# Optimization experiments

Hardware: AMD Instinct MI355X
Metric: run time of the kernel (lower is better)

The kernel has to match this reference:

```python
import jax, jax.numpy as jnp
import numpy as np

D_MODEL = 4096
NUM_EXPERTS = 64
TOP_K = 8


def setup_inputs() -> dict:
    key = jax.random.key(0)
    kx, kw = jax.random.split(key)
    x = jax.random.normal(kx, (4, 4096, D_MODEL), dtype=jnp.float32)
    # nn.Linear weight [num_experts, d_model]; y = x @ W.T
    W = jax.random.normal(kw, (NUM_EXPERTS, D_MODEL), dtype=jnp.float32) * (1.0 / np.sqrt(D_MODEL))
    return {"x": x, "W": W}


def reference(x, W):
    # logits: [b, s, e]
    logits = jnp.einsum('bsd,ed->bse', x, W)
    router_probs = jax.nn.softmax(logits, axis=-1)
    top_k_weights, top_k_indices = jax.lax.top_k(router_probs, TOP_K)
    top_k_weights = top_k_weights / (jnp.sum(top_k_weights, axis=-1, keepdims=True) + 1e-9)
    return top_k_weights, top_k_indices, router_probs
```

## Files before the change

kernel.cpp:

```cpp
#include <hip/hip_runtime.h>
#include <math.h>

#define D_MODEL 4096
#define NEXP    64
#define TOPK    8
#define NTOK    16384
#define BLK_TOK 64
#define DC      128
#define NCHUNK  (D_MODEL / DC)

#define WT2_FLOATS (NEXP * D_MODEL)

__global__ void transpose_w_kernel(const float* __restrict__ W, float* __restrict__ WT2) {
    int o = blockIdx.x * 256 + threadIdx.x;
    int j = o & 7;
    int d = (o >> 3) & (D_MODEL - 1);
    int g = o >> 15;
    WT2[o] = W[(size_t)(g * 8 + j) * D_MODEL + d];
}

__global__ __launch_bounds__(512)
void router_kernel(const float* __restrict__ x, const float* __restrict__ WT2,
                   float* __restrict__ out_w, float* __restrict__ out_i,
                   float* __restrict__ out_p, int* __restrict__ cnt,
                   int* __restrict__ list) {
    __shared__ float lds_x[2][DC / 4][BLK_TOK][4];

    const int tid  = threadIdx.x;
    const int lane = tid & 63;
    const int g    = __builtin_amdgcn_readfirstlane(tid >> 6);
    const int tok0 = blockIdx.x * BLK_TOK;

    const int row = tid >> 3;
    const int q   = tid & 7;

    float acc[8];
#pragma unroll
    for (int j = 0; j < 8; ++j) acc[j] = 0.f;

    float4 xr[4];
    const float* xbase = x + (size_t)(tok0 + row) * D_MODEL + q * 4;
    const float* wk    = WT2 + (g << 15);

    auto load_chunk = [&](int d0) {
#pragma unroll
        for (int j = 0; j < 4; ++j)
            xr[j] = *(const float4*)(xbase + d0 + j * 32);
    };
    auto store_chunk = [&](int buf) {
#pragma unroll
        for (int j = 0; j < 4; ++j)
            *(float4*)&lds_x[buf][q + j * 8][row][0] = xr[j];
    };
    auto compute_chunk = [&](int buf, int k) {
        const float* wc = wk + k * DC * 8;
        const float* xl = &lds_x[buf][0][lane][0];
#pragma unroll 4
        for (int d4 = 0; d4 < DC / 4; ++d4) {
            const float4 xq = *(const float4*)(xl + d4 * (BLK_TOK * 4));
            const float* wd = wc + d4 * 32;
#pragma unroll
            for (int dd = 0; dd < 4; ++dd) {
                const float xv = (dd == 0) ? xq.x : (dd == 1) ? xq.y : (dd == 2) ? xq.z : xq.w;
#pragma unroll
                for (int j = 0; j < 8; ++j)
                    acc[j] = fmaf(xv, wd[dd * 8 + j], acc[j]);
            }
        }
    };

    load_chunk(0);
    store_chunk(0);
    __syncthreads();

    for (int k = 0; k < NCHUNK; ++k) {
        if (k + 1 < NCHUNK) load_chunk((k + 1) * DC);
        compute_chunk(k & 1, k);
        if (k + 1 < NCHUNK) store_chunk((k + 1) & 1);
        __syncthreads();
    }

    float* lg = (float*)lds_x;
#pragma unroll
    for (int j = 0; j < 8; ++j)
        lg[lane * 65 + g * 8 + j] = acc[j];
    __syncthreads();

    if (tid < 64) {
        const int tok = tok0 + tid;
        float p[64];
        float m = -INFINITY;
#pragma unroll
        for (int e = 0; e < 64; ++e) {
            p[e] = lg[tid * 65 + e];
            m = fmaxf(m, p[e]);
        }
        float z = 0.f;
#pragma unroll
        for (int e = 0; e < 64; ++e) {
            p[e] = __expf(p[e] - m);
            z += p[e];
        }
        const float rz = 1.f / z;
#pragma unroll
        for (int e = 0; e < 64; ++e) {
            p[e] *= rz;
            lg[tid * 65 + e] = p[e];
        }

        float tv[9]; int ti[9];
#pragma unroll
        for (int k = 0; k < 9; ++k) { tv[k] = -1.f; ti[k] = 0; }
        for (int e = 0; e < 64; ++e) {
            float v = p[e]; int idx = e;
#pragma unroll
            for (int k = 0; k < 9; ++k) {
                const bool gt = v > tv[k];
                const float nv = gt ? v : tv[k];
                const int   ni = gt ? idx : ti[k];
                const float ov = gt ? tv[k] : v;
                const int   oi = gt ? ti[k] : idx;
                tv[k] = nv; ti[k] = ni; v = ov; idx = oi;
            }
        }
        int flag = 0;
#pragma unroll
        for (int k = 0; k < 8; ++k)
            if (tv[k] - tv[k + 1] <= tv[k] * 2e-4f + 1e-12f) flag = 1;
        if (flag) {
            int s = atomicAdd(cnt, 1);
            list[s] = tok;
        }

        float s8 = 0.f;
#pragma unroll
        for (int k = 0; k < 8; ++k) s8 += tv[k];
        const float denom = s8 + 1e-9f;
#pragma unroll
        for (int k = 0; k < 8; ++k) {
            out_w[tok * TOPK + k] = tv[k] / denom;
            out_i[tok * TOPK + k] = (float)ti[k];
        }
    }
    __syncthreads();

    for (int i = tid; i < BLK_TOK * 16; i += 512) {
        const int t  = i >> 4;
        const int e4 = (i & 15) << 2;
        const float* src = &lg[t * 65 + e4];
        float4 v = make_float4(src[0], src[1], src[2], src[3]);
        *(float4*)&out_p[(size_t)(tok0 + t) * NEXP + e4] = v;
    }
}

__global__ __launch_bounds__(64)
void repair_kernel(const float* __restrict__ x, const float* __restrict__ W,
                   const int* __restrict__ cnt, const int* __restrict__ list,
                   float* __restrict__ out_w, float* __restrict__ out_i) {
    __shared__ float  xs[D_MODEL];
    __shared__ double ls[NEXP];
    const int tid = threadIdx.x;
    const int n   = cnt[0];

    for (int i = blockIdx.x; i < n; i += gridDim.x) {
        const int tok = list[i];
        __syncthreads();
        const float4* xsrc = (const float4*)(x + (size_t)tok * D_MODEL);
        for (int v = tid; v < D_MODEL / 4; v += 64)
            ((float4*)xs)[v] = xsrc[v];
        __syncthreads();

        const float* wrow = W + (size_t)tid * D_MODEL;
        double s0 = 0., s1 = 0., s2 = 0., s3 = 0.;
        for (int d = 0; d < D_MODEL; d += 4) {
            const float4 wv = *(const float4*)(wrow + d);
            const float4 xv = *(const float4*)(xs + d);
            s0 += (double)xv.x * (double)wv.x;
            s1 += (double)xv.y * (double)wv.y;
            s2 += (double)xv.z * (double)wv.z;
            s3 += (double)xv.w * (double)wv.w;
        }
        ls[tid] = (s0 + s1) + (s2 + s3);
        __syncthreads();

        if (tid == 0) {
            double m = -1e300;
            for (int e = 0; e < 64; ++e) m = ls[e] > m ? ls[e] : m;
            double p[64], Z = 0.;
            for (int e = 0; e < 64; ++e) { p[e] = exp(ls[e] - m); Z += p[e]; }
            for (int e = 0; e < 64; ++e) p[e] /= Z;

            double tv[8]; int ti[8];
            for (int k = 0; k < 8; ++k) { tv[k] = -1.; ti[k] = 0; }
            for (int e = 0; e < 64; ++e) {
                double v = p[e]; int idx = e;
                for (int k = 0; k < 8; ++k) {
                    const bool gt = v > tv[k];
                    const double nv = gt ? v : tv[k];
                    const int    ni = gt ? idx : ti[k];
                    const double ov = gt ? tv[k] : v;
                    const int    oi = gt ? ti[k] : idx;
                    tv[k] = nv; ti[k] = ni; v = ov; idx = oi;
                }
            }
            double s8 = 0.;
            for (int k = 0; k < 8; ++k) s8 += tv[k];
            const double denom = s8 + 1e-9;
            for (int k = 0; k < 8; ++k) {
                out_w[tok * TOPK + k] = (float)(tv[k] / denom);
                out_i[tok * TOPK + k] = (float)ti[k];
            }
        }
    }
}

extern "C" void kernel_launch(void* const* d_in, const int* in_sizes, int n_in,
                              void* d_out, int out_size, void* d_ws, size_t ws_size,
                              hipStream_t stream) {
    const float* x = (const float*)d_in[0];
    const float* W = (const float*)d_in[1];

    float* WT2  = (float*)d_ws;
    int*   cnt  = (int*)((float*)d_ws + WT2_FLOATS);
    int*   list = cnt + 1;

    float* out   = (float*)d_out;
    float* out_w = out;
    float* out_i = out + NTOK * TOPK;
    float* out_p = out + 2 * NTOK * TOPK;

    hipMemsetAsync(cnt, 0, sizeof(int), stream);
    transpose_w_kernel<<<(WT2_FLOATS) / 256, 256, 0, stream>>>(W, WT2);
    router_kernel<<<NTOK / BLK_TOK, 512, 0, stream>>>(x, WT2, out_w, out_i, out_p, cnt, list);
    repair_kernel<<<256, 64, 0, stream>>>(x, W, cnt, list, out_w, out_i);
}
```

Baseline: 658.1 us.

## Split router GEMM over K with atomic logit accumulation and separate finalize kernel

Splits the reduction dimension in two so twice as many blocks run, and each block has 16 waves handling 4 experts each. Partial logits are summed into the probability output buffer with float atomics, and softmax and top-k move to a new finalize kernel. The LDS layout is XOR-swizzled, the inner loop uses packed 2-wide FMAs, and the repair kernel splits each dot product across four waves. In exchange it adds a memset of the output buffer, an extra kernel launch, and atomic traffic on the logits.

Result: slower. 1.478 ms (+124.5%).

```diff
diff --git a/kernel.cpp b/kernel.cpp
--- a/kernel.cpp
+++ b/kernel.cpp
@@ -7,65 +7,76 @@
 #define NTOK    16384
 #define BLK_TOK 64
 #define DC      128
-#define NCHUNK  (D_MODEL / DC)
+#define KSPLIT  2
+#define KHALF   (D_MODEL / KSPLIT)
+#define NCHUNK_H (KHALF / DC)
+#define EPW     4
+#define NWAVE   (NEXP / EPW)
+#define NTHR    (NWAVE * 64)
 
 #define WT2_FLOATS (NEXP * D_MODEL)
+
+typedef float v2f __attribute__((ext_vector_type(2)));
 
 __global__ void transpose_w_kernel(const float* __restrict__ W, float* __restrict__ WT2) {
     int o = blockIdx.x * 256 + threadIdx.x;
-    int j = o & 7;
-    int d = (o >> 3) & (D_MODEL - 1);
-    int g = o >> 15;
-    WT2[o] = W[(size_t)(g * 8 + j) * D_MODEL + d];
-}
-
-__global__ __launch_bounds__(512)
+    int p  = o & 1;
+    int j  = (o >> 1) & 3;
+    int d2 = (o >> 3) & 2047;
+    int g  = o >> 14;
+    WT2[o] = W[(size_t)(g * 4 + j) * D_MODEL + 2 * d2 + p];
+}
+
+__global__ __launch_bounds__(NTHR, 8)
 void router_kernel(const float* __restrict__ x, const float* __restrict__ WT2,
-                   float* __restrict__ out_w, float* __restrict__ out_i,
-                   float* __restrict__ out_p, int* __restrict__ cnt,
-                   int* __restrict__ list) {
-    __shared__ float lds_x[2][DC / 4][BLK_TOK][4];
+                   float* __restrict__ Pacc) {
+    __shared__ __align__(16) float lds[2 * 8192];
 
     const int tid  = threadIdx.x;
     const int lane = tid & 63;
     const int g    = __builtin_amdgcn_readfirstlane(tid >> 6);
-    const int tok0 = blockIdx.x * BLK_TOK;
-
-    const int row = tid >> 3;
-    const int q   = tid & 7;
-
-    float acc[8];
-#pragma unroll
-    for (int j = 0; j < 8; ++j) acc[j] = 0.f;
-
-    float4 xr[4];
-    const float* xbase = x + (size_t)(tok0 + row) * D_MODEL + q * 4;
-    const float* wk    = WT2 + (g << 15);
+    const int s    = blockIdx.x & 1;
+    const int tok0 = (blockIdx.x >> 1) * BLK_TOK;
+    const int kbase = s * KHALF;
+
+    const int row  = tid >> 4;
+    const int q    = tid & 15;
+    const int rowX = row ^ (q & 7);
+
+    v2f acc2[EPW];
+#pragma unroll
+    for (int j = 0; j < EPW; ++j) acc2[j] = (v2f)0.f;
+
+    float4 xr[2];
+    const float* xbase = x + (size_t)(tok0 + row) * D_MODEL + kbase + q * 4;
+    const float* wk    = WT2 + (g << 14);
 
     auto load_chunk = [&](int d0) {
 #pragma unroll
-        for (int j = 0; j < 4; ++j)
-            xr[j] = *(const float4*)(xbase + d0 + j * 32);
+        for (int j = 0; j < 2; ++j)
+            xr[j] = *(const float4*)(xbase + d0 + j * 64);
     };
     auto store_chunk = [&](int buf) {
 #pragma unroll
-        for (int j = 0; j < 4; ++j)
-            *(float4*)&lds_x[buf][q + j * 8][row][0] = xr[j];
+        for (int j = 0; j < 2; ++j)
+            *(float4*)&lds[buf * 8192 + (q + j * 16) * 256 + rowX * 4] = xr[j];
     };
-    auto compute_chunk = [&](int buf, int k) {
-        const float* wc = wk + k * DC * 8;
-        const float* xl = &lds_x[buf][0][lane][0];
-#pragma unroll 4
+    auto compute_chunk = [&](int buf, int kk) {
+        const float* wc = wk + (kbase / 2 + kk * (DC / 2)) * 8;
+        const float* xb = &lds[buf * 8192];
+#pragma unroll
         for (int d4 = 0; d4 < DC / 4; ++d4) {
-            const float4 xq = *(const float4*)(xl + d4 * (BLK_TOK * 4));
-            const float* wd = wc + d4 * 32;
-#pragma unroll
-            for (int dd = 0; dd < 4; ++dd) {
-                const float xv = (dd == 0) ? xq.x : (dd == 1) ? xq.y : (dd == 2) ? xq.z : xq.w;
-#pragma unroll
-                for (int j = 0; j < 8; ++j)
-                    acc[j] = fmaf(xv, wd[dd * 8 + j], acc[j]);
-            }
+            const int c = d4 & 7;
+            const float4 xq = *(const float4*)(xb + d4 * 256 + ((lane ^ c) << 2));
+            const float* wd = wc + d4 * 16;
+            const v2f xlo = {xq.x, xq.y};
+            const v2f xhi = {xq.z, xq.w};
+#pragma unroll
+            for (int j = 0; j < EPW; ++j)
+                acc2[j] = __builtin_elementwise_fma(xlo, *(const v2f*)(wd + j * 2), acc2[j]);
+#pragma unroll
+            for (int j = 0; j < EPW; ++j)
+                acc2[j] = __builtin_elementwise_fma(xhi, *(const v2f*)(wd + 8 + j * 2), acc2[j]);
         }
     };
 
@@ -73,17 +84,43 @@
     store_chunk(0);
     __syncthreads();
 
-    for (int k = 0; k < NCHUNK; ++k) {
-        if (k + 1 < NCHUNK) load_chunk((k + 1) * DC);
-        compute_chunk(k & 1, k);
-        if (k + 1 < NCHUNK) store_chunk((k + 1) & 1);
-        __syncthreads();
-    }
-
-    float* lg = (float*)lds_x;
-#pragma unroll
-    for (int j = 0; j < 8; ++j)
-        lg[lane * 65 + g * 8 + j] = acc[j];
+    for (int kk = 0; kk < NCHUNK_H; ++kk) {
+        if (kk + 1 < NCHUNK_H) load_chunk((kk + 1) * DC);
+        compute_chunk(kk & 1, kk);
+        if (kk + 1 < NCHUNK_H) store_chunk((kk + 1) & 1);
+        __syncthreads();
+    }
+
+    float* lg = lds;
+#pragma unroll
+    for (int j = 0; j < EPW; ++j)
+        lg[lane * 65 + g * EPW + j] = acc2[j].x + acc2[j].y;
+    __syncthreads();
+
+    {
+        const int t  = tid >> 4;
+        const int e4 = (tid & 15) << 2;
+        const float* src = &lg[t * 65 + e4];
+        float* dst = &Pacc[(size_t)(tok0 + t) * NEXP + e4];
+#pragma unroll
+        for (int c = 0; c < 4; ++c) atomicAdd(dst + c, src[c]);
+    }
+}
+
+__global__ __launch_bounds__(256)
+void finalize_kernel(float* out_p, float* __restrict__ out_w, float* __restrict__ out_i,
+                     int* __restrict__ cnt, int* __restrict__ list) {
+    __shared__ float lg[BLK_TOK * 65];
+    const int tid  = threadIdx.x;
+    const int tok0 = blockIdx.x * BLK_TOK;
+
+    for (int i = tid; i < BLK_TOK * 16; i += 256) {
+        const int t  = i >> 4;
+        const int e4 = (i & 15) << 2;
+        const float4 a = *(const float4*)&out_p[(size_t)(tok0 + t) * NEXP + e4];
+        float* dst = &lg[t * 65 + e4];
+        dst[0] = a.x; dst[1] = a.y; dst[2] = a.z; dst[3] = a.w;
+    }
     __syncthreads();
 
     if (tid < 64) {
@@ -128,8 +165,8 @@
         for (int k = 0; k < 8; ++k)
             if (tv[k] - tv[k + 1] <= tv[k] * 2e-4f + 1e-12f) flag = 1;
         if (flag) {
-            int s = atomicAdd(cnt, 1);
-            list[s] = tok;
+            int sidx = atomicAdd(cnt, 1);
+            list[sidx] = tok;
         }
 
         float s8 = 0.f;
@@ -144,63 +181,69 @@
     }
     __syncthreads();
 
-    for (int i = tid; i < BLK_TOK * 16; i += 512) {
+    for (int i = tid; i < BLK_TOK * 16; i += 256) {
         const int t  = i >> 4;
         const int e4 = (i & 15) << 2;
         const float* src = &lg[t * 65 + e4];
-        float4 v = make_float4(src[0], src[1], src[2], src[3]);
-        *(float4*)&out_p[(size_t)(tok0 + t) * NEXP + e4] = v;
-    }
-}
-
-__global__ __launch_bounds__(64)
+        *(float4*)&out_p[(size_t)(tok0 + t) * NEXP + e4] =
+            make_float4(src[0], src[1], src[2], src[3]);
+    }
+}
+
+__global__ __launch_bounds__(256)
 void repair_kernel(const float* __restrict__ x, const float* __restrict__ W,
                    const int* __restrict__ cnt, const int* __restrict__ list,
                    float* __restrict__ out_w, float* __restrict__ out_i) {
     __shared__ float  xs[D_MODEL];
-    __shared__ double ls[NEXP];
+    __shared__ double ls[4][NEXP];
     const int tid = threadIdx.x;
+    const int e   = tid & 63;
+    const int w4  = tid >> 6;
     const int n   = cnt[0];
 
     for (int i = blockIdx.x; i < n; i += gridDim.x) {
         const int tok = list[i];
         __syncthreads();
         const float4* xsrc = (const float4*)(x + (size_t)tok * D_MODEL);
-        for (int v = tid; v < D_MODEL / 4; v += 64)
+        for (int v = tid; v < D_MODEL / 4; v += 256)
             ((float4*)xs)[v] = xsrc[v];
         __syncthreads();
 
-        const float* wrow = W + (size_t)tid * D_MODEL;
+        const float* wrow = W + (size_t)e * D_MODEL + w4 * (D_MODEL / 4);
+        const float* xrow = xs + w4 * (D_MODEL / 4);
         double s0 = 0., s1 = 0., s2 = 0., s3 = 0.;
-        for (int d = 0; d < D_MODEL; d += 4) {
+        for (int d = 0; d < D_MODEL / 4; d += 4) {
             const float4 wv = *(const float4*)(wrow + d);
-            const float4 xv = *(const float4*)(xs + d);
+            const float4 xv = *(const float4*)(xrow + d);
             s0 += (double)xv.x * (double)wv.x;
             s1 += (double)xv.y * (double)wv.y;
             s2 += (double)xv.z * (double)wv.z;
             s3 += (double)xv.w * (double)wv.w;
         }
-        ls[tid] = (s0 + s1) + (s2 + s3);
+        ls[w4][e] = (s0 + s1) + (s2 + s3);
         __syncthreads();
 
         if (tid == 0) {
+            double lsum[64];
+            for (int k = 0; k < 64; ++k)
+                lsum[k] = (ls[0][k] + ls[1][k]) + (ls[2][k] + ls[3][k]);
             double m = -1e300;
-            for (int e = 0; e < 64; ++e) m = ls[e] > m ? ls[e] : m;
+            for (int k = 0; k < 64; ++k) m = lsum[k] > m ? lsum[k] : m;
             double p[64], Z = 0.;
-            for (int e = 0; e < 64; ++e) { p[e] = exp(ls[e] - m); Z += p[e]; }
-            for (int e = 0; e < 64; ++e) p[e] /= Z;
+            for (int k = 0; k < 64; ++k) { p[k] = exp(lsum[k] - m); Z += p[k]; }
+            for (int k = 0; k < 64; ++k) p[k] /= Z;
 
             double tv[8]; int ti[8];
             for (int k = 0; k < 8; ++k) { tv[k] = -1.; ti[k] = 0; }
-            for (int e = 0; e < 64; ++e) {
-                double v = p[e]; int idx = e;
-                for (int k = 0; k < 8; ++k) {
-                    const bool gt = v > tv[k];
-                    const double nv = gt ? v : tv[k];
-                    const int    ni = gt ? idx : ti[k];
-                    const double ov = gt ? tv[k] : v;
-                    const int    oi = gt ? ti[k] : idx;
-                    tv[k] = nv; ti[k] = ni; v = ov; idx = oi;
+            for (int k = 0; k < 64; ++k) {
+                double v = p[k]; int idx = k;
+                for (int u = 0; u < 8; ++u) {
+                    const bool gt = v > tv[u];
+                    const double nv = gt ? v : tv[u];
+                    const int    ni = gt ? idx : ti[u];
+                    const double ov = gt ? tv[u] : v;
+                    const int    oi = gt ? ti[u] : idx;
+                    tv[u] = nv; ti[u] = ni; v = ov; idx = oi;
                 }
             }
             double s8 = 0.;
@@ -230,7 +273,9 @@
     float* out_p = out + 2 * NTOK * TOPK;
 
     hipMemsetAsync(cnt, 0, sizeof(int), stream);
-    transpose_w_kernel<<<(WT2_FLOATS) / 256, 256, 0, stream>>>(W, WT2);
-    router_kernel<<<NTOK / BLK_TOK, 512, 0, stream>>>(x, WT2, out_w, out_i, out_p, cnt, list);
-    repair_kernel<<<256, 64, 0, stream>>>(x, W, cnt, list, out_w, out_i);
-}
+    hipMemsetAsync(out_p, 0, (size_t)NTOK * NEXP * sizeof(float), stream);
+    transpose_w_kernel<<<WT2_FLOATS / 256, 256, 0, stream>>>(W, WT2);
+    router_kernel<<<(NTOK / BLK_TOK) * KSPLIT, NTHR, 0, stream>>>(x, WT2, out_p);
+    finalize_kernel<<<NTOK / BLK_TOK, 256, 0, stream>>>(out_p, out_w, out_i, cnt, list);
+    repair_kernel<<<256, 256, 0, stream>>>(x, W, cnt, list, out_w, out_i);
+}
```
